# Kernel tuning notes

Measured on AMD Instinct MI355X. Metric: run time of the kernel, lower is better.

## Reference

```python
import jax, jax.numpy as jnp
import numpy as np

K = 7          # involution kernel size
GC = 16        # group_channels
BN_EPS = 1e-5


def conv1x1(x, w, b):
    # x: [b,c,h,w], w: [o,c], b: [o]
    return jnp.einsum('bchw,oc->bohw', x, w) + b[None, :, None, None]


def involution(x, w1, b1, w2, b2):
    # x: [b,c,h,w]; stride=1, kernel K, padding K//2
    b_, c, h, w = x.shape
    g = c // GC
    # per-pixel kernel weights: conv1x1 -> conv1x1 (no activation, as in source)
    wgt = conv1x1(conv1x1(x, w1, b1), w2, b2).reshape(b_, g, K * K, h, w)
    # patches: [b, c*K*K, h, w] with channel-major (c, kh, kw) ordering, matching torch Unfold
    pat = jax.lax.conv_general_dilated_patches(
        x, (K, K), (1, 1), ((K // 2, K // 2), (K // 2, K // 2)))
    pat = pat.reshape(b_, g, GC, K * K, h, w)
    out = jnp.einsum('bgkhw,bgckhw->bgchw', wgt, pat)
    return out.reshape(b_, c, h, w)


def hswish(x):
    return x * jnp.clip(x + 3.0, 0.0, 6.0) / 6.0


def setup_inputs() -> dict:
    key = jax.random.key(0)
    ks = jax.random.split(key, 20)
    inp, oup, mip = 256, 256, 64
    n, h, w = 16, 96, 96
    rr = 4  # involution reduction_ratio

    def rn(k, shape, s=0.05):
        return (jax.random.normal(k, shape) * s).astype(jnp.float32)

    def invp(k0, k1, k2, k3):
        return (rn(k0, (mip // rr, mip)), rn(k1, (mip // rr,)),
                rn(k2, (K * K * (mip // GC), mip // rr)),
                rn(k3, (K * K * (mip // GC),)))

    d = {}
    d['x'] = jax.random.normal(ks[0], (n, inp, h, w), dtype=jnp.float32)
    d['w_c1'] = rn(ks[1], (mip, inp)); d['b_c1'] = rn(ks[2], (mip,))
    d['inv1_w1'], d['inv1_b1'], d['inv1_w2'], d['inv1_b2'] = invp(ks[3], ks[4], ks[5], ks[6])
    d['bn_g'] = jnp.ones(mip, jnp.float32); d['bn_b'] = jnp.zeros(mip, jnp.float32)
    d['bn_m'] = jnp.zeros(mip, jnp.float32); d['bn_v'] = jnp.ones(mip, jnp.float32)
    d['invh_w1'], d['invh_b1'], d['invh_w2'], d['invh_b2'] = invp(ks[7], ks[8], ks[9], ks[10])
    d['w_h'] = rn(ks[11], (oup, mip)); d['b_h'] = rn(ks[12], (oup,))
    d['invw_w1'], d['invw_b1'], d['invw_w2'], d['invw_b2'] = invp(ks[13], ks[14], ks[15], ks[16])
    d['w_w'] = rn(ks[17], (oup, mip)); d['b_w'] = rn(ks[18], (oup,))
    return d


def reference(x, w_c1, b_c1, inv1_w1, inv1_b1, inv1_w2, inv1_b2,
              bn_g, bn_b, bn_m, bn_v,
              invh_w1, invh_b1, invh_w2, invh_b2, w_h, b_h,
              invw_w1, invw_b1, invw_w2, invw_b2, w_w, b_w):
    n, c, h, w = x.shape
    x_h = jnp.mean(x, axis=3, keepdims=True)                        # [n,c,h,1]
    x_w = jnp.mean(x, axis=2, keepdims=True).transpose(0, 1, 3, 2)  # [n,c,w,1]
    y = jnp.concatenate([x_h, x_w], axis=2)                          # [n,c,h+w,1]
    y = conv1x1(y, w_c1, b_c1)                                       # [n,mip,h+w,1]
    y = involution(y, inv1_w1, inv1_b1, inv1_w2, inv1_b2)
    inv_std = jax.lax.rsqrt(bn_v + BN_EPS)
    y = (y - bn_m[None, :, None, None]) * (bn_g * inv_std)[None, :, None, None] + bn_b[None, :, None, None]
    y = hswish(y)
    y_h = y[:, :, :h, :]                                             # [n,mip,h,1]
    y_w = y[:, :, h:, :].transpose(0, 1, 3, 2)                       # [n,mip,1,w]
    a_h = jax.nn.sigmoid(conv1x1(involution(y_h, invh_w1, invh_b1, invh_w2, invh_b2), w_h, b_h))
    a_w = jax.nn.sigmoid(conv1x1(involution(y_w, invw_w1, invw_b1, invw_w2, invw_b2), w_w, b_w))
    return x * a_w * a_h
```

## Files before the change

kernel.cpp:

```cpp
#include <hip/hip_runtime.h>
#include <math.h>

#define N_B   16
#define C_IN  256
#define MIP   64
#define HW    96
#define PTOT  192
#define KK    7

__global__ void pool_kernel(const float* __restrict__ x, float* __restrict__ pooled) {
    int plane = blockIdx.x;
    const float* xp = x + (size_t)plane * (HW * HW);
    __shared__ float sm[HW * 97];
    int t = threadIdx.x;
    #pragma unroll
    for (int k = 0; k < 9; ++k) {
        int idx = t + k * 256;
        float4 v = ((const float4*)xp)[idx];
        int flat = idx * 4;
        int row = flat / HW;
        int col = flat - row * HW;
        float* d = &sm[row * 97 + col];
        d[0] = v.x; d[1] = v.y; d[2] = v.z; d[3] = v.w;
    }
    __syncthreads();
    if (t < HW) {
        float rs = 0.f, cs = 0.f;
        #pragma unroll 4
        for (int j = 0; j < HW; ++j) rs += sm[t * 97 + j];
        #pragma unroll 4
        for (int i = 0; i < HW; ++i) cs += sm[i * 97 + t];
        float* pp = pooled + (size_t)plane * PTOT;
        pp[t]      = rs * (1.f / 96.f);
        pp[HW + t] = cs * (1.f / 96.f);
    }
}

__global__ void mid1_kernel(const float* __restrict__ pooled,
                            const float* __restrict__ w_c1, const float* __restrict__ b_c1,
                            const float* __restrict__ w1,   const float* __restrict__ b1,
                            const float* __restrict__ w2,   const float* __restrict__ b2,
                            const float* __restrict__ bn_g, const float* __restrict__ bn_b,
                            const float* __restrict__ bn_m, const float* __restrict__ bn_v,
                            float* __restrict__ y) {
    int p = blockIdx.x;
    int n = blockIdx.y;
    __shared__ float lpool[C_IN * KK];
    __shared__ float ly0[KK][MIP];
    __shared__ float lt[16];
    __shared__ float lwgt[28];
    int t = threadIdx.x;
    const float* pn = pooled + (size_t)n * C_IN * PTOT;

    #pragma unroll
    for (int it = 0; it < 7; ++it) {
        int flat = t + it * 256;
        int c = flat / KK, k = flat - (flat / KK) * KK;
        int pp = p + k - 3;
        lpool[flat] = (pp >= 0 && pp < PTOT) ? pn[c * PTOT + pp] : 0.f;
    }
    __syncthreads();

    for (int rep = 0; rep < 2; ++rep) {
        int idx = t + rep * 256;
        if (idx < MIP * KK) {
            int o = idx / KK, k = idx - o * KK;
            int pp = p + k - 3;
            float acc = 0.f;
            if (pp >= 0 && pp < PTOT) {
                const float* wrow = w_c1 + o * C_IN;
                #pragma unroll 8
                for (int c = 0; c < C_IN; ++c) acc += wrow[c] * lpool[c * KK + k];
                acc += b_c1[o];
            }
            ly0[k][o] = acc;
        }
    }
    __syncthreads();

    if (t < 16) {
        float acc = b1[t];
        const float* wr = w1 + t * MIP;
        #pragma unroll 8
        for (int o = 0; o < MIP; ++o) acc += wr[o] * ly0[3][o];
        lt[t] = acc;
    }
    __syncthreads();

    if (t < 28) {
        int g = t / KK, ky = t - g * KK;
        int q = g * 49 + ky * KK + 3;
        float acc = b2[q];
        const float* wr = w2 + q * 16;
        #pragma unroll
        for (int r = 0; r < 16; ++r) acc += wr[r] * lt[r];
        lwgt[t] = acc;
    }
    __syncthreads();

    if (t < MIP) {
        int g = t >> 4;
        float acc = 0.f;
        #pragma unroll
        for (int ky = 0; ky < KK; ++ky) acc += lwgt[g * KK + ky] * ly0[ky][t];
        float inv_std = rsqrtf(bn_v[t] + 1e-5f);
        float v = (acc - bn_m[t]) * (bn_g[t] * inv_std) + bn_b[t];
        float hs = v * fminf(fmaxf(v + 3.f, 0.f), 6.f) * (1.f / 6.f);
        y[((size_t)n * MIP + t) * PTOT + p] = hs;
    }
}

__global__ void mid2_kernel(const float* __restrict__ y,
                            const float* __restrict__ h_w1, const float* __restrict__ h_b1,
                            const float* __restrict__ h_w2, const float* __restrict__ h_b2,
                            const float* __restrict__ w_h,  const float* __restrict__ b_h,
                            const float* __restrict__ v_w1, const float* __restrict__ v_b1,
                            const float* __restrict__ v_w2, const float* __restrict__ v_b2,
                            const float* __restrict__ w_w,  const float* __restrict__ b_w,
                            float* __restrict__ a_h, float* __restrict__ a_w) {
    int p = blockIdx.x;
    int n = blockIdx.y;
    int side = (p >= HW) ? 1 : 0;
    int pos = side ? (p - HW) : p;
    const float* w1 = side ? v_w1 : h_w1;
    const float* b1 = side ? v_b1 : h_b1;
    const float* w2 = side ? v_w2 : h_w2;
    const float* b2 = side ? v_b2 : h_b2;
    const float* wf = side ? w_w : w_h;
    const float* bf = side ? b_w : b_h;

    __shared__ float ly[KK][MIP];
    __shared__ float lt[16];
    __shared__ float lwgt[28];
    __shared__ float lz[MIP];
    int t = threadIdx.x;
    const float* yn = y + (size_t)n * MIP * PTOT;

    for (int rep = 0; rep < 2; ++rep) {
        int idx = t + rep * 256;
        if (idx < MIP * KK) {
            int ch = idx / KK, k = idx - (idx / KK) * KK;
            int q = pos + k - 3;
            float v = 0.f;
            if (q >= 0 && q < HW) v = yn[ch * PTOT + (side ? (HW + q) : q)];
            ly[k][ch] = v;
        }
    }
    __syncthreads();

    if (t < 16) {
        float acc = b1[t];
        const float* wr = w1 + t * MIP;
        #pragma unroll 8
        for (int o = 0; o < MIP; ++o) acc += wr[o] * ly[3][o];
        lt[t] = acc;
    }
    __syncthreads();

    if (t < 28) {
        int g = t / KK, kk = t - (t / KK) * KK;
        int q = side ? (g * 49 + 21 + kk) : (g * 49 + kk * KK + 3);
        float acc = b2[q];
        const float* wr = w2 + q * 16;
        #pragma unroll
        for (int r = 0; r < 16; ++r) acc += wr[r] * lt[r];
        lwgt[t] = acc;
    }
    __syncthreads();

    if (t < MIP) {
        int g = t >> 4;
        float acc = 0.f;
        #pragma unroll
        for (int k = 0; k < KK; ++k) acc += lwgt[g * KK + k] * ly[k][t];
        lz[t] = acc;
    }
    __syncthreads();

    {
        int co = t;
        const float* wr = wf + co * MIP;
        float acc = bf[co];
        #pragma unroll 8
        for (int ch = 0; ch < MIP; ++ch) acc += wr[ch] * lz[ch];
        float a = 1.f / (1.f + __expf(-acc));
        float* dst = side ? a_w : a_h;
        dst[((size_t)n * C_IN + co) * HW + pos] = a;
    }
}

__global__ void apply_kernel(const float* __restrict__ x,
                             const float* __restrict__ a_h, const float* __restrict__ a_w,
                             float* __restrict__ out) {
    int plane = blockIdx.x;
    const float4* xp = (const float4*)(x + (size_t)plane * (HW * HW));
    float4* op = (float4*)(out + (size_t)plane * (HW * HW));
    __shared__ float sah[HW];
    __shared__ float saw[HW];
    int t = threadIdx.x;
    if (t < HW) {
        sah[t] = a_h[(size_t)plane * HW + t];
        saw[t] = a_w[(size_t)plane * HW + t];
    }
    __syncthreads();
    #pragma unroll
    for (int k = 0; k < 9; ++k) {
        int idx = t + k * 256;
        float4 v = xp[idx];
        int row = idx / 24;
        int c4 = (idx - row * 24) * 4;
        float ah = sah[row];
        v.x *= ah * saw[c4 + 0];
        v.y *= ah * saw[c4 + 1];
        v.z *= ah * saw[c4 + 2];
        v.w *= ah * saw[c4 + 3];
        op[idx] = v;
    }
}

extern "C" void kernel_launch(void* const* d_in, const int* in_sizes, int n_in,
                              void* d_out, int out_size, void* d_ws, size_t ws_size,
                              hipStream_t stream) {
    const float* x      = (const float*)d_in[0];
    const float* w_c1   = (const float*)d_in[1];
    const float* b_c1   = (const float*)d_in[2];
    const float* i1_w1  = (const float*)d_in[3];
    const float* i1_b1  = (const float*)d_in[4];
    const float* i1_w2  = (const float*)d_in[5];
    const float* i1_b2  = (const float*)d_in[6];
    const float* bn_g   = (const float*)d_in[7];
    const float* bn_b   = (const float*)d_in[8];
    const float* bn_m   = (const float*)d_in[9];
    const float* bn_v   = (const float*)d_in[10];
    const float* ih_w1  = (const float*)d_in[11];
    const float* ih_b1  = (const float*)d_in[12];
    const float* ih_w2  = (const float*)d_in[13];
    const float* ih_b2  = (const float*)d_in[14];
    const float* w_h    = (const float*)d_in[15];
    const float* b_h    = (const float*)d_in[16];
    const float* iw_w1  = (const float*)d_in[17];
    const float* iw_b1  = (const float*)d_in[18];
    const float* iw_w2  = (const float*)d_in[19];
    const float* iw_b2  = (const float*)d_in[20];
    const float* w_w    = (const float*)d_in[21];
    const float* b_w    = (const float*)d_in[22];
    float* out = (float*)d_out;

    float* ws = (float*)d_ws;
    float* pooled = ws;
    float* y      = ws + 786432;
    float* a_h    = ws + 786432 + 196608;
    float* a_w    = ws + 786432 + 196608 + 393216;

    pool_kernel<<<dim3(N_B * C_IN), dim3(256), 0, stream>>>(x, pooled);
    mid1_kernel<<<dim3(PTOT, N_B), dim3(256), 0, stream>>>(
        pooled, w_c1, b_c1, i1_w1, i1_b1, i1_w2, i1_b2,
        bn_g, bn_b, bn_m, bn_v, y);
    mid2_kernel<<<dim3(PTOT, N_B), dim3(256), 0, stream>>>(
        y, ih_w1, ih_b1, ih_w2, ih_b2, w_h, b_h,
        iw_w1, iw_b1, iw_w2, iw_b2, w_w, b_w, a_h, a_w);
    apply_kernel<<<dim3(N_B * C_IN), dim3(256), 0, stream>>>(x, a_h, a_w, out);
}
```

Before: 433.3 us.

## Split conv1x1 into tiled conv0 kernel and transpose final weights

Moves the first 1x1 conv out of mid1 into a separate tiled kernel that computes each pooled position once, where mid1 previously recomputed it 7 times per output for the sliding window. Intermediate y layouts change to position-major, so mid1/mid2 run 64-thread blocks with coalesced loads. A prep kernel transposes the final conv weights so the mid2 output projection reads them coalesced. The pool kernel splits row and column sums across two thread groups. The cost is two extra launches and extra workspace traffic.

```diff
diff --git a/kernel.cpp b/kernel.cpp
--- a/kernel.cpp
+++ b/kernel.cpp
@@ -7,6 +7,18 @@
 #define HW    96
 #define PTOT  192
 #define KK    7
+
+__global__ void prep_kernel(const float* __restrict__ w_h, const float* __restrict__ w_w,
+                            float* __restrict__ wfT_h, float* __restrict__ wfT_w) {
+    int idx = blockIdx.x * 256 + threadIdx.x;
+    int sel = idx >> 14;
+    int rem = idx & 16383;
+    int co = rem >> 6;
+    int ch = rem & 63;
+    const float* src = sel ? w_w : w_h;
+    float* dst = sel ? wfT_w : wfT_h;
+    dst[ch * C_IN + co] = src[co * MIP + ch];
+}
 
 __global__ void pool_kernel(const float* __restrict__ x, float* __restrict__ pooled) {
     int plane = blockIdx.x;
@@ -24,20 +36,70 @@
         d[0] = v.x; d[1] = v.y; d[2] = v.z; d[3] = v.w;
     }
     __syncthreads();
+    float* pp = pooled + (size_t)plane * PTOT;
     if (t < HW) {
-        float rs = 0.f, cs = 0.f;
+        float rs = 0.f;
         #pragma unroll 4
         for (int j = 0; j < HW; ++j) rs += sm[t * 97 + j];
+        pp[t] = rs * (1.f / 96.f);
+    } else if (t < 2 * HW) {
+        int c = t - HW;
+        float cs = 0.f;
         #pragma unroll 4
-        for (int i = 0; i < HW; ++i) cs += sm[i * 97 + t];
-        float* pp = pooled + (size_t)plane * PTOT;
-        pp[t]      = rs * (1.f / 96.f);
-        pp[HW + t] = cs * (1.f / 96.f);
-    }
-}
-
-__global__ void mid1_kernel(const float* __restrict__ pooled,
-                            const float* __restrict__ w_c1, const float* __restrict__ b_c1,
+        for (int i = 0; i < HW; ++i) cs += sm[i * 97 + c];
+        pp[HW + c] = cs * (1.f / 96.f);
+    }
+}
+
+__global__ void conv0_kernel(const float* __restrict__ pooled,
+                             const float* __restrict__ w_c1, const float* __restrict__ b_c1,
+                             float* __restrict__ y0) {
+    int p0 = blockIdx.x * 16;
+    int n  = blockIdx.y;
+    int t  = threadIdx.x;
+    __shared__ float pt[C_IN * 16];
+    __shared__ float sw[64 * 65];
+    const float* pn = pooled + (size_t)n * C_IN * PTOT;
+
+    #pragma unroll
+    for (int i = 0; i < 16; ++i) {
+        int flat = t + 256 * i;
+        int c = flat >> 4, pl = flat & 15;
+        pt[flat] = pn[c * PTOT + p0 + pl];
+    }
+
+    int o = t & 63;
+    int pl0 = (t >> 6) * 4;
+    float acc0 = 0.f, acc1 = 0.f, acc2 = 0.f, acc3 = 0.f;
+
+    for (int c0 = 0; c0 < C_IN; c0 += 64) {
+        __syncthreads();
+        #pragma unroll
+        for (int i = 0; i < 16; ++i) {
+            int flat = t + 256 * i;
+            int oo = flat >> 6, cc = flat & 63;
+            sw[oo * 65 + cc] = w_c1[oo * C_IN + c0 + cc];
+        }
+        __syncthreads();
+        #pragma unroll 8
+        for (int cc = 0; cc < 64; ++cc) {
+            float wv = sw[o * 65 + cc];
+            const float4 pv = *(const float4*)&pt[(c0 + cc) * 16 + pl0];
+            acc0 += wv * pv.x;
+            acc1 += wv * pv.y;
+            acc2 += wv * pv.z;
+            acc3 += wv * pv.w;
+        }
+    }
+    float b = b_c1[o];
+    size_t base = ((size_t)n * PTOT + p0 + pl0) * MIP + o;
+    y0[base]            = acc0 + b;
+    y0[base + MIP]      = acc1 + b;
+    y0[base + 2 * MIP]  = acc2 + b;
+    y0[base + 3 * MIP]  = acc3 + b;
+}
+
+__global__ void mid1_kernel(const float* __restrict__ y0,
                             const float* __restrict__ w1,   const float* __restrict__ b1,
                             const float* __restrict__ w2,   const float* __restrict__ b2,
                             const float* __restrict__ bn_g, const float* __restrict__ bn_b,
@@ -45,36 +107,16 @@
                             float* __restrict__ y) {
     int p = blockIdx.x;
     int n = blockIdx.y;
-    __shared__ float lpool[C_IN * KK];
+    int t = threadIdx.x;
     __shared__ float ly0[KK][MIP];
     __shared__ float lt[16];
     __shared__ float lwgt[28];
-    int t = threadIdx.x;
-    const float* pn = pooled + (size_t)n * C_IN * PTOT;
-
-    #pragma unroll
-    for (int it = 0; it < 7; ++it) {
-        int flat = t + it * 256;
-        int c = flat / KK, k = flat - (flat / KK) * KK;
+    const float* yn = y0 + (size_t)n * PTOT * MIP;
+
+    #pragma unroll
+    for (int k = 0; k < KK; ++k) {
         int pp = p + k - 3;
-        lpool[flat] = (pp >= 0 && pp < PTOT) ? pn[c * PTOT + pp] : 0.f;
-    }
-    __syncthreads();
-
-    for (int rep = 0; rep < 2; ++rep) {
-        int idx = t + rep * 256;
-        if (idx < MIP * KK) {
-            int o = idx / KK, k = idx - o * KK;
-            int pp = p + k - 3;
-            float acc = 0.f;
-            if (pp >= 0 && pp < PTOT) {
-                const float* wrow = w_c1 + o * C_IN;
-                #pragma unroll 8
-                for (int c = 0; c < C_IN; ++c) acc += wrow[c] * lpool[c * KK + k];
-                acc += b_c1[o];
-            }
-            ly0[k][o] = acc;
-        }
+        ly0[k][t] = (pp >= 0 && pp < PTOT) ? yn[pp * MIP + t] : 0.f;
     }
     __syncthreads();
 
@@ -98,7 +140,7 @@
     }
     __syncthreads();
 
-    if (t < MIP) {
+    {
         int g = t >> 4;
         float acc = 0.f;
         #pragma unroll
@@ -106,45 +148,42 @@
         float inv_std = rsqrtf(bn_v[t] + 1e-5f);
         float v = (acc - bn_m[t]) * (bn_g[t] * inv_std) + bn_b[t];
         float hs = v * fminf(fmaxf(v + 3.f, 0.f), 6.f) * (1.f / 6.f);
-        y[((size_t)n * MIP + t) * PTOT + p] = hs;
+        y[((size_t)n * PTOT + p) * MIP + t] = hs;
     }
 }
 
 __global__ void mid2_kernel(const float* __restrict__ y,
                             const float* __restrict__ h_w1, const float* __restrict__ h_b1,
                             const float* __restrict__ h_w2, const float* __restrict__ h_b2,
-                            const float* __restrict__ w_h,  const float* __restrict__ b_h,
+                            const float* __restrict__ wfT_h, const float* __restrict__ b_h,
                             const float* __restrict__ v_w1, const float* __restrict__ v_b1,
                             const float* __restrict__ v_w2, const float* __restrict__ v_b2,
-                            const float* __restrict__ w_w,  const float* __restrict__ b_w,
+                            const float* __restrict__ wfT_w, const float* __restrict__ b_w,
                             float* __restrict__ a_h, float* __restrict__ a_w) {
     int p = blockIdx.x;
     int n = blockIdx.y;
+    int t = threadIdx.x;
     int side = (p >= HW) ? 1 : 0;
     int pos = side ? (p - HW) : p;
     const float* w1 = side ? v_w1 : h_w1;
     const float* b1 = side ? v_b1 : h_b1;
     const float* w2 = side ? v_w2 : h_w2;
     const float* b2 = side ? v_b2 : h_b2;
-    const float* wf = side ? w_w : w_h;
+    const float* wf = side ? wfT_w : wfT_h;
     const float* bf = side ? b_w : b_h;
 
     __shared__ float ly[KK][MIP];
     __shared__ float lt[16];
     __shared__ float lwgt[28];
     __shared__ float lz[MIP];
-    int t = threadIdx.x;
-    const float* yn = y + (size_t)n * MIP * PTOT;
-
-    for (int rep = 0; rep < 2; ++rep) {
-        int idx = t + rep * 256;
-        if (idx < MIP * KK) {
-            int ch = idx / KK, k = idx - (idx / KK) * KK;
-            int q = pos + k - 3;
-            float v = 0.f;
-            if (q >= 0 && q < HW) v = yn[ch * PTOT + (side ? (HW + q) : q)];
-            ly[k][ch] = v;
-        }
+    const float* yn = y + (size_t)n * PTOT * MIP;
+
+    #pragma unroll
+    for (int k = 0; k < KK; ++k) {
+        int q = pos + k - 3;
+        float v = 0.f;
+        if (q >= 0 && q < HW) v = yn[(side ? (HW + q) : q) * MIP + t];
+        ly[k][t] = v;
     }
     __syncthreads();
 
@@ -168,7 +207,7 @@
     }
     __syncthreads();
 
-    if (t < MIP) {
+    {
         int g = t >> 4;
         float acc = 0.f;
         #pragma unroll
@@ -177,14 +216,14 @@
     }
     __syncthreads();
 
-    {
-        int co = t;
-        const float* wr = wf + co * MIP;
+    float* dst = side ? a_w : a_h;
+    #pragma unroll
+    for (int q = 0; q < 4; ++q) {
+        int co = q * 64 + t;
         float acc = bf[co];
         #pragma unroll 8
-        for (int ch = 0; ch < MIP; ++ch) acc += wr[ch] * lz[ch];
+        for (int ch = 0; ch < MIP; ++ch) acc += wf[ch * C_IN + co] * lz[ch];
         float a = 1.f / (1.f + __expf(-acc));
-        float* dst = side ? a_w : a_h;
         dst[((size_t)n * C_IN + co) * HW + pos] = a;
     }
 }
@@ -248,16 +287,20 @@
 
     float* ws = (float*)d_ws;
     float* pooled = ws;
-    float* y      = ws + 786432;
-    float* a_h    = ws + 786432 + 196608;
-    float* a_w    = ws + 786432 + 196608 + 393216;
-
+    float* y0     = pooled + 786432;
+    float* y      = y0 + 196608;
+    float* a_h    = y + 196608;
+    float* a_w    = a_h + 393216;
+    float* wfT_h  = a_w + 393216;
+    float* wfT_w  = wfT_h + 16384;
+
+    prep_kernel<<<dim3(128), dim3(256), 0, stream>>>(w_h, w_w, wfT_h, wfT_w);
     pool_kernel<<<dim3(N_B * C_IN), dim3(256), 0, stream>>>(x, pooled);
-    mid1_kernel<<<dim3(PTOT, N_B), dim3(256), 0, stream>>>(
-        pooled, w_c1, b_c1, i1_w1, i1_b1, i1_w2, i1_b2,
-        bn_g, bn_b, bn_m, bn_v, y);
-    mid2_kernel<<<dim3(PTOT, N_B), dim3(256), 0, stream>>>(
-        y, ih_w1, ih_b1, ih_w2, ih_b2, w_h, b_h,
-        iw_w1, iw_b1, iw_w2, iw_b2, w_w, b_w, a_h, a_w);
+    conv0_kernel<<<dim3(12, N_B), dim3(256), 0, stream>>>(pooled, w_c1, b_c1, y0);
+    mid1_kernel<<<dim3(PTOT, N_B), dim3(64), 0, stream>>>(
+        y0, i1_w1, i1_b1, i1_w2, i1_b2, bn_g, bn_b, bn_m, bn_v, y);
+    mid2_kernel<<<dim3(PTOT, N_B), dim3(64), 0, stream>>>(
+        y, ih_w1, ih_b1, ih_w2, ih_b2, wfT_h, b_h,
+        iw_w1, iw_b1, iw_w2, iw_b2, wfT_w, b_w, a_h, a_w);
     apply_kernel<<<dim3(N_B * C_IN), dim3(256), 0, stream>>>(x, a_h, a_w, out);
 }
```

Measured after the change: 359.9 us. -16.9%, faster.
